# Performance work log

Measured on AMD Instinct MI355X. Metric: run time of the kernel, lower is better.

Reference implementation:

```python
import jax, jax.numpy as jnp
import numpy as np

N_NODES = 100000


def _gcn_conv(x, row, col, ew, W, b, n):
    # PyG GCNConv: add self-loops (weight 1), symmetric normalization,
    # linear transform, scatter-add aggregation at target, then bias.
    loop = jnp.arange(n, dtype=row.dtype)
    r = jnp.concatenate([row, loop])
    c = jnp.concatenate([col, loop])
    w = jnp.concatenate([ew, jnp.ones((n,), ew.dtype)])
    deg = jax.ops.segment_sum(w, c, num_segments=n)
    dinv = jnp.where(deg > 0, jax.lax.rsqrt(deg), 0.0)
    nrm = dinv[r] * w * dinv[c]                 # [E+N]
    h = x @ W                                    # [N, out]
    msg = h[r] * nrm[:, None]                    # gather + scale
    return jax.ops.segment_sum(msg, c, num_segments=n) + b


def setup_inputs() -> dict:
    key = jax.random.key(0)
    ks = jax.random.split(key, 16)
    n, e, f, s = N_NODES, 1600000, 8, 64
    return {
        "x": jax.random.normal(ks[0], (n, f), jnp.float32),
        "edge_index": jax.random.randint(ks[1], (2, e), 0, n, jnp.int32),
        "edge_weight": jax.random.uniform(ks[2], (e,), jnp.float32),
        "s_values": jax.random.normal(ks[3], (s,), jnp.float32),
        "s_fc1_w": jax.random.normal(ks[4], (s, s // 2), jnp.float32) * 0.1,
        "s_fc1_b": jax.random.normal(ks[5], (s // 2,), jnp.float32) * 0.1,
        "s_fc2_w": jax.random.normal(ks[6], (s // 2, 1), jnp.float32) * 0.1,
        "s_fc2_b": jax.random.normal(ks[7], (1,), jnp.float32) * 0.1,
        "conv1_w": jax.random.normal(ks[8], (f + 1, 32), jnp.float32) * 0.3,
        "conv1_b": jax.random.normal(ks[9], (32,), jnp.float32) * 0.1,
        "conv2_w": jax.random.normal(ks[10], (32, 16), jnp.float32) * 0.2,
        "conv2_b": jax.random.normal(ks[11], (16,), jnp.float32) * 0.1,
        "fc1_w": jax.random.normal(ks[12], (16, 1), jnp.float32) * 0.25,
        "fc1_b": jax.random.normal(ks[13], (1,), jnp.float32) * 0.1,
    }


def reference(x, edge_index, edge_weight, s_values,
              s_fc1_w, s_fc1_b, s_fc2_w, s_fc2_b,
              conv1_w, conv1_b, conv2_w, conv2_b, fc1_w, fc1_b):
    n = x.shape[0]
    row, col = edge_index[0], edge_index[1]
    # s-value encoder: two small linears, ReLU between
    s_enc = jax.nn.relu(s_values @ s_fc1_w + s_fc1_b) @ s_fc2_w + s_fc2_b  # [1]
    xs = jnp.concatenate([x, jnp.broadcast_to(s_enc[None, :], (n, 1))], axis=1)
    h1 = _gcn_conv(xs, row, col, edge_weight, conv1_w, conv1_b, n)
    h1 = jax.nn.leaky_relu(h1, 0.01)
    # dropout is identity in eval mode; norm=False skips GraphNorm
    h2 = _gcn_conv(h1, row, col, edge_weight, conv2_w, conv2_b, n)
    h2 = jax.nn.leaky_relu(h2, 0.01)
    return h2 @ fc1_w + fc1_b  # [N, 1]
```

## Files before the change

### kernel.cpp

```cpp
#include <hip/hip_runtime.h>
#include <hip/hip_fp16.h>


#define NBLKA  256
#define BSH    7
#define BNODES 128
#define MAXBK  784

__global__ void k_senc(const float* __restrict__ sv, const float* __restrict__ w1,
                       const float* __restrict__ b1, const float* __restrict__ w2,
                       const float* __restrict__ b2, float* __restrict__ senc) {
    __shared__ float hid[32];
    int j = threadIdx.x;
    if (j < 32) {
        float acc = b1[j];
        #pragma unroll 8
        for (int k = 0; k < 64; ++k) acc += sv[k] * w1[k * 32 + j];
        hid[j] = acc > 0.f ? acc : 0.f;
    }
    __syncthreads();
    if (j == 0) {
        float acc = b2[0];
        #pragma unroll 8
        for (int k = 0; k < 32; ++k) acc += hid[k] * w2[k];
        senc[0] = acc;
    }
}

__global__ void k_hist(const int* __restrict__ ei, int* __restrict__ hist,
                       int E, int EPB, int NBK) {
    __shared__ int lh[MAXBK];
    for (int k = threadIdx.x; k < NBK; k += blockDim.x) lh[k] = 0;
    __syncthreads();
    int b = blockIdx.x;
    int e0 = b * EPB, e1 = min(E, e0 + EPB);
    for (int e = e0 + threadIdx.x; e < e1; e += blockDim.x)
        atomicAdd(&lh[ei[E + e] >> BSH], 1);
    __syncthreads();
    for (int k = threadIdx.x; k < NBK; k += blockDim.x)
        hist[(size_t)k * NBLKA + b] = lh[k];
}

__global__ void k_scan1(int* __restrict__ data, int* __restrict__ bsum, int nflat) {
    __shared__ int s[512];
    int i = blockIdx.x * 512 + threadIdx.x;
    int v = (i < nflat) ? data[i] : 0;
    s[threadIdx.x] = v;
    __syncthreads();
    for (int off = 1; off < 512; off <<= 1) {
        int tv = (threadIdx.x >= off) ? s[threadIdx.x - off] : 0;
        __syncthreads();
        if (threadIdx.x >= off) s[threadIdx.x] += tv;
        __syncthreads();
    }
    if (i < nflat) data[i] = s[threadIdx.x] - v;
    if (threadIdx.x == 511) bsum[blockIdx.x] = s[511];
}

__global__ void k_scan2(int* __restrict__ bsum, int nb) {
    __shared__ int s[512];
    __shared__ int carry;
    if (threadIdx.x == 0) carry = 0;
    __syncthreads();
    for (int base = 0; base < nb; base += 512) {
        int idx = base + threadIdx.x;
        int v = (idx < nb) ? bsum[idx] : 0;
        s[threadIdx.x] = v;
        __syncthreads();
        for (int off = 1; off < 512; off <<= 1) {
            int tv = (threadIdx.x >= off) ? s[threadIdx.x - off] : 0;
            __syncthreads();
            if (threadIdx.x >= off) s[threadIdx.x] += tv;
            __syncthreads();
        }
        if (idx < nb) bsum[idx] = s[threadIdx.x] - v + carry;
        __syncthreads();
        if (threadIdx.x == 0) carry += s[511];
        __syncthreads();
    }
}

__global__ void k_scan3(int* __restrict__ data, const int* __restrict__ bsum, int nflat) {
    int i = blockIdx.x * 512 + threadIdx.x;
    if (i < nflat) data[i] += bsum[i >> 9];
}

__global__ void k_scatter(const int* __restrict__ ei, const float* __restrict__ ew,
                          const int* __restrict__ scanned, int2* __restrict__ ebuf,
                          int E, int EPB, int NBK) {
    __shared__ int lbase[MAXBK];
    int b = blockIdx.x;
    for (int k = threadIdx.x; k < NBK; k += blockDim.x)
        lbase[k] = scanned[(size_t)k * NBLKA + b];
    __syncthreads();
    int e0 = b * EPB, e1 = min(E, e0 + EPB);
    for (int e = e0 + threadIdx.x; e < e1; e += blockDim.x) {
        int c = ei[E + e];
        int r = ei[e];
        int k = c >> BSH;
        int pos = atomicAdd(&lbase[k], 1);
        ebuf[pos] = make_int2(r | ((c & (BNODES - 1)) << 25), __float_as_int(ew[e]));
    }
}

__global__ void k_sort(const int* __restrict__ scanned, const int2* __restrict__ ebuf,
                       int* __restrict__ row, float* __restrict__ dinv,
                       int2* __restrict__ csr, int n, int E, int NBK) {
    __shared__ int lcnt[BNODES];
    __shared__ int lofs[BNODES];
    __shared__ float lw[BNODES];
    int k = blockIdx.x;
    if (threadIdx.x < BNODES) { lcnt[threadIdx.x] = 0; lw[threadIdx.x] = 1.0f; }
    __syncthreads();
    int bs = scanned[(size_t)k * NBLKA];
    int be = (k + 1 < NBK) ? scanned[(size_t)(k + 1) * NBLKA] : E;
    for (int s = bs + threadIdx.x; s < be; s += blockDim.x) {
        int2 ent = ebuf[s];
        int cl = ((unsigned)ent.x) >> 25;
        atomicAdd(&lcnt[cl], 1);
        atomicAdd(&lw[cl], __int_as_float(ent.y));
    }
    __syncthreads();
    int v = (threadIdx.x < BNODES) ? lcnt[threadIdx.x] : 0;
    if (threadIdx.x < BNODES) lofs[threadIdx.x] = v;
    __syncthreads();
    for (int off = 1; off < BNODES; off <<= 1) {
        int tv = 0;
        if (threadIdx.x < BNODES && threadIdx.x >= off) tv = lofs[threadIdx.x - off];
        __syncthreads();
        if (threadIdx.x < BNODES && threadIdx.x >= off) lofs[threadIdx.x] += tv;
        __syncthreads();
    }
    if (threadIdx.x < BNODES) {
        int excl = lofs[threadIdx.x] - v;
        lofs[threadIdx.x] = excl;
        int i = k * BNODES + threadIdx.x;
        if (i < n) {
            row[i] = bs + excl;
            dinv[i] = rsqrtf(lw[threadIdx.x]);
        }
    }
    if (k == NBK - 1 && threadIdx.x == 0) row[n] = E;
    __syncthreads();
    for (int s = bs + threadIdx.x; s < be; s += blockDim.x) {
        int2 ent = ebuf[s];
        int cl = ((unsigned)ent.x) >> 25;
        int pos = bs + atomicAdd(&lofs[cl], 1);
        csr[pos] = make_int2(ent.x & 0x01FFFFFF, ent.y);
    }
}

__global__ void k_prep(int2* __restrict__ csr, const float* __restrict__ dinv, int E) {
    int e = blockIdx.x * blockDim.x + threadIdx.x;
    if (e >= E) return;
    int2 ent = csr[e];
    ent.y = __float_as_int(__int_as_float(ent.y) * dinv[ent.x]);
    csr[e] = ent;
}

__global__ void k_xh(const float* __restrict__ x, __half* __restrict__ xh, int n) {
    int i = blockIdx.x * blockDim.x + threadIdx.x;
    if (i >= n) return;
    const float4* xi = reinterpret_cast<const float4*>(x + (size_t)i * 8);
    float4 u = xi[0], v = xi[1];
    __half2 h0 = __floats2half2_rn(u.x, u.y);
    __half2 h1 = __floats2half2_rn(u.z, u.w);
    __half2 h2 = __floats2half2_rn(v.x, v.y);
    __half2 h3 = __floats2half2_rn(v.z, v.w);
    uint4 w;
    w.x = *reinterpret_cast<unsigned*>(&h0);
    w.y = *reinterpret_cast<unsigned*>(&h1);
    w.z = *reinterpret_cast<unsigned*>(&h2);
    w.w = *reinterpret_cast<unsigned*>(&h3);
    reinterpret_cast<uint4*>(xh + (size_t)i * 8)[0] = w;
}

__global__ void k_pass1(const int* __restrict__ row, const int2* __restrict__ csr,
                        const float* __restrict__ dinv, const __half* __restrict__ xh,
                        const float* __restrict__ senc,
                        const float* __restrict__ W1, const float* __restrict__ b1,
                        const float* __restrict__ W2, __half* __restrict__ th, int n) {
    __shared__ float sW1[288];
    __shared__ float sb1[32];
    __shared__ float sW2[32 * 17];
    for (int j = threadIdx.x; j < 288; j += blockDim.x) sW1[j] = W1[j];
    for (int j = threadIdx.x; j < 512; j += blockDim.x) sW2[(j >> 4) * 17 + (j & 15)] = W2[j];
    if (threadIdx.x < 32) sb1[threadIdx.x] = b1[threadIdx.x];
    __syncthreads();
    int g = blockIdx.x * blockDim.x + threadIdx.x;
    int i = g >> 2;
    int quad = g & 3;
    if (i >= n) return;
    float di = dinv[i];
    float a[8];
    float sw;
    if (quad == 0) {
        const uint4* xp = reinterpret_cast<const uint4*>(xh + (size_t)i * 8);
        uint4 w = xp[0];
        const __half2* hh = reinterpret_cast<const __half2*>(&w);
        #pragma unroll
        for (int q = 0; q < 4; ++q) {
            float2 f = __half22float2(hh[q]);
            a[2 * q] = di * f.x; a[2 * q + 1] = di * f.y;
        }
        sw = di;
    } else {
        #pragma unroll
        for (int q = 0; q < 8; ++q) a[q] = 0.f;
        sw = 0.f;
    }
    int s0 = row[i], s1 = row[i + 1];
    for (int s = s0 + quad; s < s1; s += 4) {
        int2 ent = csr[s];
        float wpre = __int_as_float(ent.y);
        const uint4* xp = reinterpret_cast<const uint4*>(xh + (size_t)ent.x * 8);
        uint4 w = xp[0];
        const __half2* hh = reinterpret_cast<const __half2*>(&w);
        #pragma unroll
        for (int q = 0; q < 4; ++q) {
            float2 f = __half22float2(hh[q]);
            a[2 * q] += wpre * f.x; a[2 * q + 1] += wpre * f.y;
        }
        sw += wpre;
    }
    #pragma unroll
    for (int q = 0; q < 8; ++q) a[q] += __shfl_xor(a[q], 1);
    sw += __shfl_xor(sw, 1);
    #pragma unroll
    for (int q = 0; q < 8; ++q) a[q] += __shfl_xor(a[q], 2);
    sw += __shfl_xor(sw, 2);
    float a8 = di * sw * senc[0];
    float af[8];
    #pragma unroll
    for (int q = 0; q < 8; ++q) af[q] = di * a[q];
    float h[8];
    #pragma unroll
    for (int jj = 0; jj < 8; ++jj) {
        int j = quad * 8 + jj;
        float acc = sb1[j] + a8 * sW1[8 * 32 + j];
        #pragma unroll
        for (int f = 0; f < 8; ++f) acc += af[f] * sW1[f * 32 + j];
        h[jj] = acc > 0.f ? acc : 0.01f * acc;
    }
    float p[16];
    #pragma unroll
    for (int o = 0; o < 16; ++o) p[o] = 0.f;
    #pragma unroll
    for (int jj = 0; jj < 8; ++jj) {
        int j = quad * 8 + jj;
        #pragma unroll
        for (int o = 0; o < 16; ++o) p[o] += h[jj] * sW2[j * 17 + o];
    }
    #pragma unroll
    for (int o = 0; o < 16; ++o) p[o] += __shfl_xor(p[o], 1);
    #pragma unroll
    for (int o = 0; o < 16; ++o) p[o] += __shfl_xor(p[o], 2);
    int o0 = quad * 4;
    __half2 hv0 = __floats2half2_rn(p[o0 + 0], p[o0 + 1]);
    __half2 hv1 = __floats2half2_rn(p[o0 + 2], p[o0 + 3]);
    uint2 st;
    st.x = *reinterpret_cast<unsigned*>(&hv0);
    st.y = *reinterpret_cast<unsigned*>(&hv1);
    reinterpret_cast<uint2*>(th + (size_t)i * 16 + o0)[0] = st;
}

__global__ void k_pass2(const int* __restrict__ row, const int2* __restrict__ csr,
                        const float* __restrict__ dinv, const __half* __restrict__ th,
                        const float* __restrict__ b2, const float* __restrict__ fw,
                        const float* __restrict__ fb, float* __restrict__ out, int n) {
    __shared__ float sb2[16];
    __shared__ float sfw[16];
    if (threadIdx.x < 16) { sb2[threadIdx.x] = b2[threadIdx.x]; sfw[threadIdx.x] = fw[threadIdx.x]; }
    __syncthreads();
    int g = blockIdx.x * blockDim.x + threadIdx.x;
    int i = g >> 2;
    int quad = g & 3;
    if (i >= n) return;
    float di = dinv[i];
    float acc[16];
    if (quad == 0) {
        const uint4* tp = reinterpret_cast<const uint4*>(th + (size_t)i * 16);
        uint4 w0 = tp[0], w1 = tp[1];
        const __half2* hh0 = reinterpret_cast<const __half2*>(&w0);
        const __half2* hh1 = reinterpret_cast<const __half2*>(&w1);
        #pragma unroll
        for (int q = 0; q < 4; ++q) {
            float2 f0 = __half22float2(hh0[q]);
            float2 f1 = __half22float2(hh1[q]);
            acc[2 * q + 0] = di * f0.x; acc[2 * q + 1] = di * f0.y;
            acc[8 + 2 * q + 0] = di * f1.x; acc[8 + 2 * q + 1] = di * f1.y;
        }
    } else {
        #pragma unroll
        for (int q = 0; q < 16; ++q) acc[q] = 0.f;
    }
    int s0 = row[i], s1 = row[i + 1];
    for (int s = s0 + quad; s < s1; s += 4) {
        int2 ent = csr[s];
        float wpre = __int_as_float(ent.y);
        const uint4* tp = reinterpret_cast<const uint4*>(th + (size_t)ent.x * 16);
        uint4 w0 = tp[0], w1 = tp[1];
        const __half2* hh0 = reinterpret_cast<const __half2*>(&w0);
        const __half2* hh1 = reinterpret_cast<const __half2*>(&w1);
        #pragma unroll
        for (int q = 0; q < 4; ++q) {
            float2 f0 = __half22float2(hh0[q]);
            float2 f1 = __half22float2(hh1[q]);
            acc[2 * q + 0] += wpre * f0.x; acc[2 * q + 1] += wpre * f0.y;
            acc[8 + 2 * q + 0] += wpre * f1.x; acc[8 + 2 * q + 1] += wpre * f1.y;
        }
    }
    #pragma unroll
    for (int q = 0; q < 16; ++q) acc[q] += __shfl_xor(acc[q], 1);
    #pragma unroll
    for (int q = 0; q < 16; ++q) acc[q] += __shfl_xor(acc[q], 2);
    if (quad) return;
    float o = fb[0];
    #pragma unroll
    for (int q = 0; q < 16; ++q) {
        float v = di * acc[q] + sb2[q];
        v = v > 0.f ? v : 0.01f * v;
        o += v * sfw[q];
    }
    out[i] = o;
}

extern "C" void kernel_launch(void* const* d_in, const int* in_sizes, int n_in,
                              void* d_out, int out_size, void* d_ws, size_t ws_size,
                              hipStream_t stream) {
    const float* x      = (const float*)d_in[0];
    const int*   ei     = (const int*)d_in[1];
    const float* ew     = (const float*)d_in[2];
    const float* sv     = (const float*)d_in[3];
    const float* sfc1w  = (const float*)d_in[4];
    const float* sfc1b  = (const float*)d_in[5];
    const float* sfc2w  = (const float*)d_in[6];
    const float* sfc2b  = (const float*)d_in[7];
    const float* conv1w = (const float*)d_in[8];
    const float* conv1b = (const float*)d_in[9];
    const float* conv2w = (const float*)d_in[10];
    const float* conv2b = (const float*)d_in[11];
    const float* fc1w   = (const float*)d_in[12];
    const float* fc1b   = (const float*)d_in[13];

    const int n = in_sizes[0] / 8;
    const int E = in_sizes[2];

    const int NBK   = (n + BNODES - 1) >> BSH;
    const int nflat = NBK * NBLKA;
    const int EPB   = (E + NBLKA - 1) / NBLKA;
    const int nb1   = (nflat + 511) / 512;

    size_t off = 0;
    auto alloc = [&](size_t words) { size_t o = off; off += (words + 3) & ~(size_t)3; return o; };
    float*  base = (float*)d_ws;
    float*  senc = base + alloc(4);
    float*  dinv = base + alloc(n);
    int*    rowp = (int*)(base + alloc(n + 1));
    int*    hist = (int*)(base + alloc(nflat));
    int*    bsum = (int*)(base + alloc(512));
    int2*   ebuf = (int2*)(base + alloc((size_t)2 * E));
    int2*   csr  = (int2*)(base + alloc((size_t)2 * E));
    __half* xh   = (__half*)(base + alloc((size_t)4 * n));
    __half* th   = (__half*)(base + alloc((size_t)8 * n));

    const int BT = 256;
    const int gN = (n + BT - 1) / BT;
    const int gE = (E + BT - 1) / BT;
    const int g4 = ((size_t)4 * n + BT - 1) / BT;

    k_senc<<<1, 64, 0, stream>>>(sv, sfc1w, sfc1b, sfc2w, sfc2b, senc);
    k_xh<<<gN, BT, 0, stream>>>(x, xh, n);
    k_hist<<<NBLKA, 1024, 0, stream>>>(ei, hist, E, EPB, NBK);
    k_scan1<<<nb1, 512, 0, stream>>>(hist, bsum, nflat);
    k_scan2<<<1, 512, 0, stream>>>(bsum, nb1);
    k_scan3<<<nb1, 512, 0, stream>>>(hist, bsum, nflat);
    k_scatter<<<NBLKA, 1024, 0, stream>>>(ei, ew, hist, ebuf, E, EPB, NBK);
    k_sort<<<NBK, 512, 0, stream>>>(hist, ebuf, rowp, dinv, csr, n, E, NBK);
    k_prep<<<gE, BT, 0, stream>>>(csr, dinv, E);
    k_pass1<<<g4, BT, 0, stream>>>(rowp, csr, dinv, xh, senc,
                                   conv1w, conv1b, conv2w, th, n);
    k_pass2<<<g4, BT, 0, stream>>>(rowp, csr, dinv, th,
                                   conv2b, fc1w, fc1b, (float*)d_out, n);
}
```

Measured before the change: 116.4 us.

## Pack CSR entries into 32 bits and fold small kernels into neighbours

CSR entries shrink from an int2 to a single 32-bit word holding a 17-bit source index and a 15-bit half-precision weight with the sign bit dropped. This halves CSR traffic in prep and in both aggregation passes. The s-encoder moves into an extra block of the xh conversion kernel, and the scan3 pass is removed by adding the block sums inline where scatter and sort read offsets, which saves two launches. The packing assumes fewer than 131072 nodes and non-negative weights, and storing weights in half precision costs accuracy.

```diff
diff --git a/kernel.cpp b/kernel.cpp
--- a/kernel.cpp
+++ b/kernel.cpp
@@ -7,158 +7,35 @@
 #define BNODES 128
 #define MAXBK  784
 
-__global__ void k_senc(const float* __restrict__ sv, const float* __restrict__ w1,
-                       const float* __restrict__ b1, const float* __restrict__ w2,
-                       const float* __restrict__ b2, float* __restrict__ senc) {
-    __shared__ float hid[32];
-    int j = threadIdx.x;
-    if (j < 32) {
-        float acc = b1[j];
-        #pragma unroll 8
-        for (int k = 0; k < 64; ++k) acc += sv[k] * w1[k * 32 + j];
-        hid[j] = acc > 0.f ? acc : 0.f;
-    }
-    __syncthreads();
-    if (j == 0) {
-        float acc = b2[0];
-        #pragma unroll 8
-        for (int k = 0; k < 32; ++k) acc += hid[k] * w2[k];
-        senc[0] = acc;
-    }
-}
-
-__global__ void k_hist(const int* __restrict__ ei, int* __restrict__ hist,
-                       int E, int EPB, int NBK) {
-    __shared__ int lh[MAXBK];
-    for (int k = threadIdx.x; k < NBK; k += blockDim.x) lh[k] = 0;
-    __syncthreads();
-    int b = blockIdx.x;
-    int e0 = b * EPB, e1 = min(E, e0 + EPB);
-    for (int e = e0 + threadIdx.x; e < e1; e += blockDim.x)
-        atomicAdd(&lh[ei[E + e] >> BSH], 1);
-    __syncthreads();
-    for (int k = threadIdx.x; k < NBK; k += blockDim.x)
-        hist[(size_t)k * NBLKA + b] = lh[k];
-}
-
-__global__ void k_scan1(int* __restrict__ data, int* __restrict__ bsum, int nflat) {
-    __shared__ int s[512];
-    int i = blockIdx.x * 512 + threadIdx.x;
-    int v = (i < nflat) ? data[i] : 0;
-    s[threadIdx.x] = v;
-    __syncthreads();
-    for (int off = 1; off < 512; off <<= 1) {
-        int tv = (threadIdx.x >= off) ? s[threadIdx.x - off] : 0;
-        __syncthreads();
-        if (threadIdx.x >= off) s[threadIdx.x] += tv;
-        __syncthreads();
-    }
-    if (i < nflat) data[i] = s[threadIdx.x] - v;
-    if (threadIdx.x == 511) bsum[blockIdx.x] = s[511];
-}
-
-__global__ void k_scan2(int* __restrict__ bsum, int nb) {
-    __shared__ int s[512];
-    __shared__ int carry;
-    if (threadIdx.x == 0) carry = 0;
-    __syncthreads();
-    for (int base = 0; base < nb; base += 512) {
-        int idx = base + threadIdx.x;
-        int v = (idx < nb) ? bsum[idx] : 0;
-        s[threadIdx.x] = v;
-        __syncthreads();
-        for (int off = 1; off < 512; off <<= 1) {
-            int tv = (threadIdx.x >= off) ? s[threadIdx.x - off] : 0;
-            __syncthreads();
-            if (threadIdx.x >= off) s[threadIdx.x] += tv;
-            __syncthreads();
-        }
-        if (idx < nb) bsum[idx] = s[threadIdx.x] - v + carry;
-        __syncthreads();
-        if (threadIdx.x == 0) carry += s[511];
-        __syncthreads();
-    }
-}
-
-__global__ void k_scan3(int* __restrict__ data, const int* __restrict__ bsum, int nflat) {
-    int i = blockIdx.x * 512 + threadIdx.x;
-    if (i < nflat) data[i] += bsum[i >> 9];
-}
-
-__global__ void k_scatter(const int* __restrict__ ei, const float* __restrict__ ew,
-                          const int* __restrict__ scanned, int2* __restrict__ ebuf,
-                          int E, int EPB, int NBK) {
-    __shared__ int lbase[MAXBK];
-    int b = blockIdx.x;
-    for (int k = threadIdx.x; k < NBK; k += blockDim.x)
-        lbase[k] = scanned[(size_t)k * NBLKA + b];
-    __syncthreads();
-    int e0 = b * EPB, e1 = min(E, e0 + EPB);
-    for (int e = e0 + threadIdx.x; e < e1; e += blockDim.x) {
-        int c = ei[E + e];
-        int r = ei[e];
-        int k = c >> BSH;
-        int pos = atomicAdd(&lbase[k], 1);
-        ebuf[pos] = make_int2(r | ((c & (BNODES - 1)) << 25), __float_as_int(ew[e]));
-    }
-}
-
-__global__ void k_sort(const int* __restrict__ scanned, const int2* __restrict__ ebuf,
-                       int* __restrict__ row, float* __restrict__ dinv,
-                       int2* __restrict__ csr, int n, int E, int NBK) {
-    __shared__ int lcnt[BNODES];
-    __shared__ int lofs[BNODES];
-    __shared__ float lw[BNODES];
-    int k = blockIdx.x;
-    if (threadIdx.x < BNODES) { lcnt[threadIdx.x] = 0; lw[threadIdx.x] = 1.0f; }
-    __syncthreads();
-    int bs = scanned[(size_t)k * NBLKA];
-    int be = (k + 1 < NBK) ? scanned[(size_t)(k + 1) * NBLKA] : E;
-    for (int s = bs + threadIdx.x; s < be; s += blockDim.x) {
-        int2 ent = ebuf[s];
-        int cl = ((unsigned)ent.x) >> 25;
-        atomicAdd(&lcnt[cl], 1);
-        atomicAdd(&lw[cl], __int_as_float(ent.y));
-    }
-    __syncthreads();
-    int v = (threadIdx.x < BNODES) ? lcnt[threadIdx.x] : 0;
-    if (threadIdx.x < BNODES) lofs[threadIdx.x] = v;
-    __syncthreads();
-    for (int off = 1; off < BNODES; off <<= 1) {
-        int tv = 0;
-        if (threadIdx.x < BNODES && threadIdx.x >= off) tv = lofs[threadIdx.x - off];
-        __syncthreads();
-        if (threadIdx.x < BNODES && threadIdx.x >= off) lofs[threadIdx.x] += tv;
-        __syncthreads();
-    }
-    if (threadIdx.x < BNODES) {
-        int excl = lofs[threadIdx.x] - v;
-        lofs[threadIdx.x] = excl;
-        int i = k * BNODES + threadIdx.x;
-        if (i < n) {
-            row[i] = bs + excl;
-            dinv[i] = rsqrtf(lw[threadIdx.x]);
-        }
-    }
-    if (k == NBK - 1 && threadIdx.x == 0) row[n] = E;
-    __syncthreads();
-    for (int s = bs + threadIdx.x; s < be; s += blockDim.x) {
-        int2 ent = ebuf[s];
-        int cl = ((unsigned)ent.x) >> 25;
-        int pos = bs + atomicAdd(&lofs[cl], 1);
-        csr[pos] = make_int2(ent.x & 0x01FFFFFF, ent.y);
-    }
-}
-
-__global__ void k_prep(int2* __restrict__ csr, const float* __restrict__ dinv, int E) {
-    int e = blockIdx.x * blockDim.x + threadIdx.x;
-    if (e >= E) return;
-    int2 ent = csr[e];
-    ent.y = __float_as_int(__int_as_float(ent.y) * dinv[ent.x]);
-    csr[e] = ent;
-}
-
-__global__ void k_xh(const float* __restrict__ x, __half* __restrict__ xh, int n) {
+__device__ inline unsigned enc_w(float w) {
+    return ((unsigned)__half_as_ushort(__float2half_rn(w)) & 0x7FFFu) << 17;
+}
+__device__ inline float dec_w(unsigned e) {
+    return __half2float(__ushort_as_half((unsigned short)((e >> 17) & 0x7FFFu)));
+}
+
+__global__ void k_xh(const float* __restrict__ x, __half* __restrict__ xh, int n,
+                     const float* __restrict__ sv, const float* __restrict__ w1,
+                     const float* __restrict__ b1, const float* __restrict__ w2,
+                     const float* __restrict__ b2, float* __restrict__ senc) {
+    if (blockIdx.x == gridDim.x - 1) {
+        __shared__ float hid[32];
+        int j = threadIdx.x;
+        if (j < 32) {
+            float acc = b1[j];
+            #pragma unroll 8
+            for (int k = 0; k < 64; ++k) acc += sv[k] * w1[k * 32 + j];
+            hid[j] = acc > 0.f ? acc : 0.f;
+        }
+        __syncthreads();
+        if (j == 0) {
+            float acc = b2[0];
+            #pragma unroll 8
+            for (int k = 0; k < 32; ++k) acc += hid[k] * w2[k];
+            senc[0] = acc;
+        }
+        return;
+    }
     int i = blockIdx.x * blockDim.x + threadIdx.x;
     if (i >= n) return;
     const float4* xi = reinterpret_cast<const float4*>(x + (size_t)i * 8);
@@ -175,7 +52,142 @@
     reinterpret_cast<uint4*>(xh + (size_t)i * 8)[0] = w;
 }
 
-__global__ void k_pass1(const int* __restrict__ row, const int2* __restrict__ csr,
+__global__ void k_hist(const int* __restrict__ ei, int* __restrict__ hist,
+                       int E, int EPB, int NBK) {
+    __shared__ int lh[MAXBK];
+    for (int k = threadIdx.x; k < NBK; k += blockDim.x) lh[k] = 0;
+    __syncthreads();
+    int b = blockIdx.x;
+    int e0 = b * EPB, e1 = min(E, e0 + EPB);
+    for (int e = e0 + threadIdx.x; e < e1; e += blockDim.x)
+        atomicAdd(&lh[ei[E + e] >> BSH], 1);
+    __syncthreads();
+    for (int k = threadIdx.x; k < NBK; k += blockDim.x)
+        hist[(size_t)k * NBLKA + b] = lh[k];
+}
+
+__global__ void k_scan1(int* __restrict__ data, int* __restrict__ bsum, int nflat) {
+    __shared__ int s[512];
+    int i = blockIdx.x * 512 + threadIdx.x;
+    int v = (i < nflat) ? data[i] : 0;
+    s[threadIdx.x] = v;
+    __syncthreads();
+    for (int off = 1; off < 512; off <<= 1) {
+        int tv = (threadIdx.x >= off) ? s[threadIdx.x - off] : 0;
+        __syncthreads();
+        if (threadIdx.x >= off) s[threadIdx.x] += tv;
+        __syncthreads();
+    }
+    if (i < nflat) data[i] = s[threadIdx.x] - v;
+    if (threadIdx.x == 511) bsum[blockIdx.x] = s[511];
+}
+
+__global__ void k_scan2(int* __restrict__ bsum, int nb) {
+    __shared__ int s[512];
+    __shared__ int carry;
+    if (threadIdx.x == 0) carry = 0;
+    __syncthreads();
+    for (int base = 0; base < nb; base += 512) {
+        int idx = base + threadIdx.x;
+        int v = (idx < nb) ? bsum[idx] : 0;
+        s[threadIdx.x] = v;
+        __syncthreads();
+        for (int off = 1; off < 512; off <<= 1) {
+            int tv = (threadIdx.x >= off) ? s[threadIdx.x - off] : 0;
+            __syncthreads();
+            if (threadIdx.x >= off) s[threadIdx.x] += tv;
+            __syncthreads();
+        }
+        if (idx < nb) bsum[idx] = s[threadIdx.x] - v + carry;
+        __syncthreads();
+        if (threadIdx.x == 0) carry += s[511];
+        __syncthreads();
+    }
+}
+
+__global__ void k_scatter(const int* __restrict__ ei, const float* __restrict__ ew,
+                          const int* __restrict__ scanned, const int* __restrict__ bsum,
+                          int2* __restrict__ ebuf, int E, int EPB, int NBK) {
+    __shared__ int lbase[MAXBK];
+    int b = blockIdx.x;
+    for (int k = threadIdx.x; k < NBK; k += blockDim.x) {
+        int idx = k * NBLKA + b;
+        lbase[k] = scanned[idx] + bsum[idx >> 9];
+    }
+    __syncthreads();
+    int e0 = b * EPB, e1 = min(E, e0 + EPB);
+    for (int e = e0 + threadIdx.x; e < e1; e += blockDim.x) {
+        int c = ei[E + e];
+        int r = ei[e];
+        int k = c >> BSH;
+        int pos = atomicAdd(&lbase[k], 1);
+        ebuf[pos] = make_int2(r | ((c & (BNODES - 1)) << 25), __float_as_int(ew[e]));
+    }
+}
+
+__global__ void k_sort(const int* __restrict__ scanned, const int* __restrict__ bsum,
+                       const int2* __restrict__ ebuf,
+                       int* __restrict__ row, float* __restrict__ dinv,
+                       unsigned* __restrict__ csr4, int n, int E, int NBK) {
+    __shared__ int lcnt[BNODES];
+    __shared__ int lofs[BNODES];
+    __shared__ float lw[BNODES];
+    int k = blockIdx.x;
+    if (threadIdx.x < BNODES) { lcnt[threadIdx.x] = 0; lw[threadIdx.x] = 1.0f; }
+    __syncthreads();
+    int idx0 = k * NBLKA;
+    int bs = scanned[idx0] + bsum[idx0 >> 9];
+    int be = E;
+    if (k + 1 < NBK) {
+        int idx1 = (k + 1) * NBLKA;
+        be = scanned[idx1] + bsum[idx1 >> 9];
+    }
+    for (int s = bs + threadIdx.x; s < be; s += blockDim.x) {
+        int2 ent = ebuf[s];
+        int cl = ((unsigned)ent.x) >> 25;
+        atomicAdd(&lcnt[cl], 1);
+        atomicAdd(&lw[cl], __int_as_float(ent.y));
+    }
+    __syncthreads();
+    int v = (threadIdx.x < BNODES) ? lcnt[threadIdx.x] : 0;
+    if (threadIdx.x < BNODES) lofs[threadIdx.x] = v;
+    __syncthreads();
+    for (int off = 1; off < BNODES; off <<= 1) {
+        int tv = 0;
+        if (threadIdx.x < BNODES && threadIdx.x >= off) tv = lofs[threadIdx.x - off];
+        __syncthreads();
+        if (threadIdx.x < BNODES && threadIdx.x >= off) lofs[threadIdx.x] += tv;
+        __syncthreads();
+    }
+    if (threadIdx.x < BNODES) {
+        int excl = lofs[threadIdx.x] - v;
+        lofs[threadIdx.x] = excl;
+        int i = k * BNODES + threadIdx.x;
+        if (i < n) {
+            row[i] = bs + excl;
+            dinv[i] = rsqrtf(lw[threadIdx.x]);
+        }
+    }
+    if (k == NBK - 1 && threadIdx.x == 0) row[n] = E;
+    __syncthreads();
+    for (int s = bs + threadIdx.x; s < be; s += blockDim.x) {
+        int2 ent = ebuf[s];
+        int cl = ((unsigned)ent.x) >> 25;
+        int pos = bs + atomicAdd(&lofs[cl], 1);
+        csr4[pos] = enc_w(__int_as_float(ent.y)) | (unsigned)(ent.x & 0x1FFFF);
+    }
+}
+
+__global__ void k_prep(unsigned* __restrict__ csr4, const float* __restrict__ dinv, int E) {
+    int e = blockIdx.x * blockDim.x + threadIdx.x;
+    if (e >= E) return;
+    unsigned ent = csr4[e];
+    unsigned src = ent & 0x1FFFFu;
+    float wpre = dec_w(ent) * dinv[src];
+    csr4[e] = enc_w(wpre) | src;
+}
+
+__global__ void k_pass1(const int* __restrict__ row, const unsigned* __restrict__ csr4,
                         const float* __restrict__ dinv, const __half* __restrict__ xh,
                         const float* __restrict__ senc,
                         const float* __restrict__ W1, const float* __restrict__ b1,
@@ -211,9 +223,9 @@
     }
     int s0 = row[i], s1 = row[i + 1];
     for (int s = s0 + quad; s < s1; s += 4) {
-        int2 ent = csr[s];
-        float wpre = __int_as_float(ent.y);
-        const uint4* xp = reinterpret_cast<const uint4*>(xh + (size_t)ent.x * 8);
+        unsigned ent = csr4[s];
+        float wpre = dec_w(ent);
+        const uint4* xp = reinterpret_cast<const uint4*>(xh + (size_t)(ent & 0x1FFFFu) * 8);
         uint4 w = xp[0];
         const __half2* hh = reinterpret_cast<const __half2*>(&w);
         #pragma unroll
@@ -264,7 +276,7 @@
     reinterpret_cast<uint2*>(th + (size_t)i * 16 + o0)[0] = st;
 }
 
-__global__ void k_pass2(const int* __restrict__ row, const int2* __restrict__ csr,
+__global__ void k_pass2(const int* __restrict__ row, const unsigned* __restrict__ csr4,
                         const float* __restrict__ dinv, const __half* __restrict__ th,
                         const float* __restrict__ b2, const float* __restrict__ fw,
                         const float* __restrict__ fb, float* __restrict__ out, int n) {
@@ -296,9 +308,9 @@
     }
     int s0 = row[i], s1 = row[i + 1];
     for (int s = s0 + quad; s < s1; s += 4) {
-        int2 ent = csr[s];
-        float wpre = __int_as_float(ent.y);
-        const uint4* tp = reinterpret_cast<const uint4*>(th + (size_t)ent.x * 16);
+        unsigned ent = csr4[s];
+        float wpre = dec_w(ent);
+        const uint4* tp = reinterpret_cast<const uint4*>(th + (size_t)(ent & 0x1FFFFu) * 16);
         uint4 w0 = tp[0], w1 = tp[1];
         const __half2* hh0 = reinterpret_cast<const __half2*>(&w0);
         const __half2* hh1 = reinterpret_cast<const __half2*>(&w1);
@@ -353,33 +365,31 @@
 
     size_t off = 0;
     auto alloc = [&](size_t words) { size_t o = off; off += (words + 3) & ~(size_t)3; return o; };
-    float*  base = (float*)d_ws;
-    float*  senc = base + alloc(4);
-    float*  dinv = base + alloc(n);
-    int*    rowp = (int*)(base + alloc(n + 1));
-    int*    hist = (int*)(base + alloc(nflat));
-    int*    bsum = (int*)(base + alloc(512));
-    int2*   ebuf = (int2*)(base + alloc((size_t)2 * E));
-    int2*   csr  = (int2*)(base + alloc((size_t)2 * E));
-    __half* xh   = (__half*)(base + alloc((size_t)4 * n));
-    __half* th   = (__half*)(base + alloc((size_t)8 * n));
+    float*    base = (float*)d_ws;
+    float*    senc = base + alloc(4);
+    float*    dinv = base + alloc(n);
+    int*      rowp = (int*)(base + alloc(n + 1));
+    int*      hist = (int*)(base + alloc(nflat));
+    int*      bsum = (int*)(base + alloc(512));
+    int2*     ebuf = (int2*)(base + alloc((size_t)2 * E));
+    unsigned* csr4 = (unsigned*)(base + alloc(E));
+    __half*   xh   = (__half*)(base + alloc((size_t)4 * n));
+    __half*   th   = (__half*)(base + alloc((size_t)8 * n));
 
     const int BT = 256;
     const int gN = (n + BT - 1) / BT;
     const int gE = (E + BT - 1) / BT;
     const int g4 = ((size_t)4 * n + BT - 1) / BT;
 
-    k_senc<<<1, 64, 0, stream>>>(sv, sfc1w, sfc1b, sfc2w, sfc2b, senc);
-    k_xh<<<gN, BT, 0, stream>>>(x, xh, n);
+    k_xh<<<gN + 1, BT, 0, stream>>>(x, xh, n, sv, sfc1w, sfc1b, sfc2w, sfc2b, senc);
     k_hist<<<NBLKA, 1024, 0, stream>>>(ei, hist, E, EPB, NBK);
     k_scan1<<<nb1, 512, 0, stream>>>(hist, bsum, nflat);
     k_scan2<<<1, 512, 0, stream>>>(bsum, nb1);
-    k_scan3<<<nb1, 512, 0, stream>>>(hist, bsum, nflat);
-    k_scatter<<<NBLKA, 1024, 0, stream>>>(ei, ew, hist, ebuf, E, EPB, NBK);
-    k_sort<<<NBK, 512, 0, stream>>>(hist, ebuf, rowp, dinv, csr, n, E, NBK);
-    k_prep<<<gE, BT, 0, stream>>>(csr, dinv, E);
-    k_pass1<<<g4, BT, 0, stream>>>(rowp, csr, dinv, xh, senc,
+    k_scatter<<<NBLKA, 1024, 0, stream>>>(ei, ew, hist, bsum, ebuf, E, EPB, NBK);
+    k_sort<<<NBK, 512, 0, stream>>>(hist, bsum, ebuf, rowp, dinv, csr4, n, E, NBK);
+    k_prep<<<gE, BT, 0, stream>>>(csr4, dinv, E);
+    k_pass1<<<g4, BT, 0, stream>>>(rowp, csr4, dinv, xh, senc,
                                    conv1w, conv1b, conv2w, th, n);
-    k_pass2<<<g4, BT, 0, stream>>>(rowp, csr, dinv, th,
+    k_pass2<<<g4, BT, 0, stream>>>(rowp, csr4, dinv, th,
                                    conv2b, fc1w, fc1b, (float*)d_out, n);
 }
```

Measured after the change: 105.3 us. -9.6%, faster.
